# Optimization experiments

Measured on AMD Instinct MI355X. Metric: run time of the kernel, lower is better.

Reference implementation:

```python
import jax, jax.numpy as jnp
import numpy as np

GROUP_SIZE = 16
E2M1_MAX = 6.0
# Positive E2M1 grid and midpoints for round-to-nearest
E2M1_POS = jnp.array([0.0, 0.5, 1.0, 1.5, 2.0, 3.0, 4.0, 6.0], jnp.float32)
E2M1_MID = jnp.array([0.25, 0.75, 1.25, 1.75, 2.5, 3.5, 5.0], jnp.float32)
# Full 16-entry signed LUT (bit3 = sign, sign-magnitude)
E2M1_LUT = jnp.array([0.0, 0.5, 1.0, 1.5, 2.0, 3.0, 4.0, 6.0,
                      -0.0, -0.5, -1.0, -1.5, -2.0, -3.0, -4.0, -6.0], jnp.float32)

def _round_e2m1(x):
    # nearest value on the E2M1 grid (clamped to +-6)
    idx = jnp.searchsorted(E2M1_MID, jnp.abs(x))
    return jnp.sign(x) * E2M1_POS[idx]

def nvfp4_act_qdq(x, input_scale):
    # per-group dynamic quantize to NVFP4 with fp8-e4m3 group scale, then dequantize
    orig_shape = x.shape
    xg = x.astype(jnp.float32).reshape(*orig_shape[:-1], -1, GROUP_SIZE)
    amax = jnp.max(jnp.abs(xg), axis=-1, keepdims=True)
    s = (amax / (E2M1_MAX * input_scale)).astype(jnp.float8_e4m3fn).astype(jnp.float32)
    s = jnp.where(s > 0, s, 1.0)
    total = s * input_scale  # effective per-group scale
    dq = _round_e2m1(xg / total) * total
    return dq.reshape(orig_shape).astype(jnp.float16)

def nvfp4_dequantize(weight, weight_scale, weight_scale_2):
    # weight: [O, I//2] packed bytes (values 0..255); low nibble = even index
    O = weight.shape[0]
    low = weight & 0xF
    high = (weight >> 4) & 0xF
    codes = jnp.stack([low, high], axis=-1).reshape(O, -1)  # [O, I]
    vals = E2M1_LUT[codes].reshape(O, -1, GROUP_SIZE)       # [O, G, 16]
    w = vals * weight_scale[:, :, None] * weight_scale_2
    return w.reshape(O, -1).astype(jnp.float16)

def setup_inputs() -> dict:
    key = jax.random.key(0)
    k1, k2, k3 = jax.random.split(key, 3)
    B, S, I, O = 8, 16, 8192, 8192
    hidden_states = jax.random.normal(k1, (B, S, I), dtype=jnp.float16)
    weight = jax.random.randint(k2, (O, I // 2), 0, 256, dtype=jnp.int32)
    weight_scale = jax.random.uniform(k3, (O, I // GROUP_SIZE), dtype=jnp.float32) * 0.05 + 0.001
    weight_scale_2 = jnp.ones((1,), jnp.float32)
    input_scale = jnp.ones((1,), jnp.float32)
    return {"hidden_states": hidden_states, "weight": weight,
            "weight_scale": weight_scale, "weight_scale_2": weight_scale_2,
            "input_scale": input_scale}

def reference(hidden_states, weight, weight_scale, weight_scale_2, input_scale):
    hs_dq = nvfp4_act_qdq(hidden_states, input_scale)
    w_dq = nvfp4_dequantize(weight, weight_scale, weight_scale_2)
    return jnp.matmul(hs_dq, w_dq.T)  # [B, S, O], fp16
```

## Files before the change

kernel.cpp:

```cpp
#include <hip/hip_runtime.h>
#include <stdint.h>


typedef _Float16 half8 __attribute__((ext_vector_type(8)));
typedef float float4v __attribute__((ext_vector_type(4)));

__device__ __forceinline__ uint32_t perm_b32(uint32_t hi, uint32_t lo, uint32_t sel) {
  return __builtin_amdgcn_perm(hi, lo, sel);
}

__device__ __forceinline__ float e4m3_roundtrip(float x) {
  if (x < 0.015625f) {
    return __builtin_rintf(x * 512.0f) * 0.001953125f;
  }
  uint32_t u = __float_as_uint(x);
  u += 0x7FFFFu + ((u >> 20) & 1u);
  u &= 0xFFF00000u;
  float y = __uint_as_float(u);
  return fminf(y, 448.0f);
}

__global__ __launch_bounds__(256)
void aqdq_kernel(const float* __restrict__ hs,
                 const float* __restrict__ isc,
                 uint2* __restrict__ asw) {
  const int t = blockIdx.x * 256 + threadIdx.x;
  const int m = t >> 11;
  const int u = t & 2047;
  const int g = u >> 2;
  const int hq = u & 3;

  const float* p = hs + m * 8192 + g * 16 + hq * 4;
  float4 x = *(const float4*)p;

  float amax = fmaxf(fmaxf(fabsf(x.x), fabsf(x.y)), fmaxf(fabsf(x.z), fabsf(x.w)));
  amax = fmaxf(amax, __shfl_xor(amax, 1));
  amax = fmaxf(amax, __shfl_xor(amax, 2));

  float is = isc[0];
  float s = e4m3_roundtrip(amax / (6.0f * is));
  if (!(s > 0.0f)) s = 1.0f;
  float total = s * is;

  float xv[4] = {x.x, x.y, x.z, x.w};
  union { _Float16 h[4]; uint2 v; } qq;
#pragma unroll
  for (int i = 0; i < 4; ++i) {
    float r = xv[i] / total;
    float a = fabsf(r);
    float v = (a <= 0.25f) ? 0.0f
            : (a <= 0.75f) ? 0.5f
            : (a <= 1.25f) ? 1.0f
            : (a <= 1.75f) ? 1.5f
            : (a <= 2.5f)  ? 2.0f
            : (a <= 3.5f)  ? 3.0f
            : (a <= 5.0f)  ? 4.0f : 6.0f;
    qq.h[i] = (_Float16)(copysignf(v, r) * total);
  }

  const int k = g * 16 + hq * 4;
  const int kb = k >> 5;
  const int quad = (k >> 3) & 3;
  const int lane16 = (m & 15) | (quad << 4);
  const int mb = m >> 4;
  asw[((kb * 8 + mb) * 64 + lane16) * 2 + (hq & 1)] = qq.v;
}

__device__ __forceinline__ half8 decode_scale(int4 w, float sf) {
  uint32_t t0 = perm_b32((uint32_t)w.y, (uint32_t)w.x, 0x00000400u);
  uint32_t t1 = perm_b32((uint32_t)w.w, (uint32_t)w.z, 0x04000000u);
  uint32_t b  = perm_b32(t1, t0, 0x07060100u);
  uint32_t ev = b & 0x0F0F0F0Fu;
  uint32_t od = (b >> 4) & 0x0F0F0F0Fu;
  uint32_t evm = ev & 0x07070707u;
  uint32_t odm = od & 0x07070707u;
  uint32_t evs = (ev & 0x08080808u) << 4;
  uint32_t ods = (od & 0x08080808u) << 4;
  uint32_t evh = perm_b32(0x46444240u, 0x3E3C3800u, evm) | evs;
  uint32_t odh = perm_b32(0x46444240u, 0x3E3C3800u, odm) | ods;
  union { uint32_t u[4]; half8 h; } r;
  r.u[0] = perm_b32(odh, evh, 0x04000000u) & 0xFF00FF00u;
  r.u[1] = perm_b32(odh, evh, 0x05000100u) & 0xFF00FF00u;
  r.u[2] = perm_b32(odh, evh, 0x06000200u) & 0xFF00FF00u;
  r.u[3] = perm_b32(odh, evh, 0x07000300u) & 0xFF00FF00u;
  _Float16 hsf = (_Float16)sf;
  half8 sv = {hsf, hsf, hsf, hsf, hsf, hsf, hsf, hsf};
  return r.h * sv;
}

template<int MODE>
__global__ __launch_bounds__(512, 4)
void gemm_kernel(const uint4* __restrict__ asw,
                 const int* __restrict__ wq,
                 const float* __restrict__ wsc,
                 const float* __restrict__ ws2p,
                 float* __restrict__ dst) {
  __shared__ uint4 abuf[2][8][64];
  const int lane = threadIdx.x & 63;
  const int wv = threadIdx.x >> 6;
  const int quad = lane >> 4;
  const int kp = blockIdx.x & 7;
  const int nb = blockIdx.x >> 3;
  const int col = nb * 128 + wv * 16 + (lane & 15);
  const float ws2 = ws2p[0];
  const int4* wp = (const int4*)(wq + (size_t)col * 4096) + kp * 128 + quad;
  const float2* sp = (const float2*)(wsc + (size_t)col * 512 + kp * 64);
  const uint4* ap = asw + kp * 16384 + wv * 64 + lane;

  float4v acc[8];
#pragma unroll
  for (int mb = 0; mb < 8; ++mb) acc[mb] = (float4v){0.f, 0.f, 0.f, 0.f};

  {
    uint4 a0 = ap[0];
    int4 w0 = wp[0];
    float2 s0 = sp[0];
    abuf[0][wv][lane] = a0;
    __syncthreads();
    int4 wC = w0; float2 sC = s0;
    for (int t = 0; t < 32; ++t) {
      uint4 aN; int4 wN; float2 sN;
      const bool more = (t < 31);
      if (more) {
        aN = ap[(t + 1) * 512];
        wN = wp[(t + 1) * 4];
        sN = sp[t + 1];
      }
      uint4 af[8];
#pragma unroll
      for (int mb = 0; mb < 8; ++mb) af[mb] = abuf[t & 1][mb][lane];
      float sA = ((quad & 2) ? sC.y : sC.x) * ws2;
      half8 bA = decode_scale(wC, sA);
#pragma unroll
      for (int mb = 0; mb < 8; ++mb) {
        union { uint4 u; half8 h; } a;
        a.u = af[mb];
        acc[mb] = __builtin_amdgcn_mfma_f32_16x16x32_f16(a.h, bA, acc[mb], 0, 0, 0);
      }
      if (more) {
        abuf[(t + 1) & 1][wv][lane] = aN;
        __syncthreads();
        wC = wN; sC = sN;
      }
    }
  }

  if (MODE == 0) {
    float* pp = dst + ((size_t)kp << 20) + col;
#pragma unroll
    for (int mb = 0; mb < 8; ++mb) {
      const int mrow = mb * 16 + quad * 4;
#pragma unroll
      for (int r = 0; r < 4; ++r) pp[(size_t)(mrow + r) * 8192] = acc[mb][r];
    }
  } else {
#pragma unroll
    for (int mb = 0; mb < 8; ++mb) {
      const int mrow = mb * 16 + quad * 4;
#pragma unroll
      for (int r = 0; r < 4; ++r)
        unsafeAtomicAdd(&dst[(size_t)(mrow + r) * 8192 + col], acc[mb][r]);
    }
  }
}

__global__ __launch_bounds__(256)
void reduce_kernel(const float4* __restrict__ part, float4* __restrict__ out) {
  const int i = blockIdx.x * 256 + threadIdx.x;
  float4 s = part[i];
#pragma unroll
  for (int p = 1; p < 8; ++p) {
    float4 b = part[(size_t)p * 262144 + i];
    s.x += b.x; s.y += b.y; s.z += b.z; s.w += b.w;
  }
  out[i] = s;
}

extern "C" void kernel_launch(void* const* d_in, const int* in_sizes, int n_in,
                              void* d_out, int out_size, void* d_ws, size_t ws_size,
                              hipStream_t stream) {
  (void)in_sizes; (void)n_in; (void)out_size;
  const float* hs  = (const float*)d_in[0];
  const int* wq    = (const int*)d_in[1];
  const float* wsc = (const float*)d_in[2];
  const float* ws2 = (const float*)d_in[3];
  const float* isc = (const float*)d_in[4];
  float* out       = (float*)d_out;
  uint2* asw2      = (uint2*)d_ws;
  const uint4* asw4 = (const uint4*)d_ws;

  aqdq_kernel<<<1024, 256, 0, stream>>>(hs, isc, asw2);

  const size_t need = ((size_t)2 << 20) + ((size_t)32 << 20);
  if (ws_size >= need) {
    float* part = (float*)((char*)d_ws + ((size_t)2 << 20));
    gemm_kernel<0><<<512, 512, 0, stream>>>(asw4, wq, wsc, ws2, part);
    reduce_kernel<<<1024, 256, 0, stream>>>((const float4*)part, (float4*)out);
  } else {
    hipMemsetAsync(out, 0, (size_t)128 * 8192 * 4, stream);
    gemm_kernel<1><<<512, 512, 0, stream>>>(asw4, wq, wsc, ws2, out);
  }
}
```

Measured before the change: 241.9 us.

## Deepen GEMM prefetch with direct global-to-LDS loads and a 4-stage ring

The activation tiles are now copied straight from global memory into LDS with global_load_lds, so they no longer pass through registers and a separate LDS store. A 4-deep LDS ring with prefetch distance 2 replaces the double buffer, with weights and scales held in a matching register ring. Explicit vmcnt waits and a single barrier per step replace the per-iteration __syncthreads, and the main loop is unrolled by four. The goal is to keep more loads in flight and hide memory latency. The cost is more LDS and registers per block, which may reduce occupancy, and the hand-counted vmcnt values, which must match exactly the number of outstanding loads.

```diff
diff --git a/kernel.cpp b/kernel.cpp
--- a/kernel.cpp
+++ b/kernel.cpp
@@ -7,6 +7,12 @@
 
 __device__ __forceinline__ uint32_t perm_b32(uint32_t hi, uint32_t lo, uint32_t sel) {
   return __builtin_amdgcn_perm(hi, lo, sel);
+}
+
+__device__ __forceinline__ void load_lds16(const uint4* g, uint4* l) {
+  __builtin_amdgcn_global_load_lds((const __attribute__((address_space(1))) void*)g,
+                                   (__attribute__((address_space(3))) void*)l,
+                                   16, 0, 0);
 }
 
 __device__ __forceinline__ float e4m3_roundtrip(float x) {
@@ -95,7 +101,7 @@
                  const float* __restrict__ wsc,
                  const float* __restrict__ ws2p,
                  float* __restrict__ dst) {
-  __shared__ uint4 abuf[2][8][64];
+  __shared__ uint4 abuf[4][8][64];
   const int lane = threadIdx.x & 63;
   const int wv = threadIdx.x >> 6;
   const int quad = lane >> 4;
@@ -111,39 +117,59 @@
 #pragma unroll
   for (int mb = 0; mb < 8; ++mb) acc[mb] = (float4v){0.f, 0.f, 0.f, 0.f};
 
+  int4 wreg[4];
+  float2 sreg[4];
+
+  load_lds16(ap, &abuf[0][wv][0]);
+  wreg[0] = wp[0];
+  sreg[0] = sp[0];
+  load_lds16(ap + 512, &abuf[1][wv][0]);
+  wreg[1] = wp[4];
+  sreg[1] = sp[1];
+
+#define STEP_BODY(J, STAGE_EN, VMCNT_N)                                           \
+  {                                                                               \
+    if (STAGE_EN) {                                                               \
+      load_lds16(apg + ((J) + 2) * 512, &abuf[((J) + 2) & 3][wv][0]);             \
+      wreg[((J) + 2) & 3] = wpg[((J) + 2) * 4];                                   \
+      sreg[((J) + 2) & 3] = spg[(J) + 2];                                         \
+    }                                                                             \
+    __builtin_amdgcn_sched_barrier(0);                                            \
+    asm volatile("s_waitcnt vmcnt(" #VMCNT_N ")" ::: "memory");                   \
+    __builtin_amdgcn_s_barrier();                                                 \
+    __builtin_amdgcn_sched_barrier(0);                                            \
+    uint4 af[8];                                                                  \
+    _Pragma("unroll")                                                             \
+    for (int mb = 0; mb < 8; ++mb) af[mb] = abuf[(J)][mb][lane];                  \
+    float sA = ((quad & 2) ? sreg[(J)].y : sreg[(J)].x) * ws2;                    \
+    half8 bA = decode_scale(wreg[(J)], sA);                                       \
+    _Pragma("unroll")                                                             \
+    for (int mb = 0; mb < 8; ++mb) {                                              \
+      union { uint4 u; half8 h; } a;                                              \
+      a.u = af[mb];                                                               \
+      acc[mb] = __builtin_amdgcn_mfma_f32_16x16x32_f16(a.h, bA, acc[mb], 0, 0, 0);\
+    }                                                                             \
+  }
+
   {
-    uint4 a0 = ap[0];
-    int4 w0 = wp[0];
-    float2 s0 = sp[0];
-    abuf[0][wv][lane] = a0;
-    __syncthreads();
-    int4 wC = w0; float2 sC = s0;
-    for (int t = 0; t < 32; ++t) {
-      uint4 aN; int4 wN; float2 sN;
-      const bool more = (t < 31);
-      if (more) {
-        aN = ap[(t + 1) * 512];
-        wN = wp[(t + 1) * 4];
-        sN = sp[t + 1];
-      }
-      uint4 af[8];
-#pragma unroll
-      for (int mb = 0; mb < 8; ++mb) af[mb] = abuf[t & 1][mb][lane];
-      float sA = ((quad & 2) ? sC.y : sC.x) * ws2;
-      half8 bA = decode_scale(wC, sA);
-#pragma unroll
-      for (int mb = 0; mb < 8; ++mb) {
-        union { uint4 u; half8 h; } a;
-        a.u = af[mb];
-        acc[mb] = __builtin_amdgcn_mfma_f32_16x16x32_f16(a.h, bA, acc[mb], 0, 0, 0);
-      }
-      if (more) {
-        abuf[(t + 1) & 1][wv][lane] = aN;
-        __syncthreads();
-        wC = wN; sC = sN;
-      }
+    const uint4* apg = ap;
+    const int4* wpg = wp;
+    const float2* spg = sp;
+    for (int tt = 0; tt < 28; tt += 4) {
+      STEP_BODY(0, true, 6)
+      STEP_BODY(1, true, 6)
+      STEP_BODY(2, true, 6)
+      STEP_BODY(3, true, 6)
+      apg += 4 * 512;
+      wpg += 16;
+      spg += 4;
     }
-  }
+    STEP_BODY(0, true, 6)
+    STEP_BODY(1, true, 6)
+    STEP_BODY(2, false, 3)
+    STEP_BODY(3, false, 0)
+  }
+#undef STEP_BODY
 
   if (MODE == 0) {
     float* pp = dst + ((size_t)kp << 20) + col;
```

Result: no change. 243.9 us (+0.8%).

## Use direct global-to-LDS loads with 4-step windows and fewer barriers in GEMM

Applied to the files above, without the earlier changes.

Activation tiles now go straight from global memory to LDS through global_load_lds, which drops the register round trip. The K loop is regrouped into 8 windows of 4 k-steps, each with double-buffered weight and scale registers, so there is one barrier per window instead of one per step. Scales are fetched as float4 vectors. In exchange, LDS use grows fourfold and register pressure rises, which could lower occupancy at 512 threads with launch bounds of 4.

```diff
diff --git a/kernel.cpp b/kernel.cpp
--- a/kernel.cpp
+++ b/kernel.cpp
@@ -7,6 +7,12 @@
 
 __device__ __forceinline__ uint32_t perm_b32(uint32_t hi, uint32_t lo, uint32_t sel) {
   return __builtin_amdgcn_perm(hi, lo, sel);
+}
+
+__device__ __forceinline__ void load_lds16(const uint4* g, uint4* l) {
+  __builtin_amdgcn_global_load_lds((const __attribute__((address_space(1))) void*)g,
+                                   (__attribute__((address_space(3))) void*)l,
+                                   16, 0, 0);
 }
 
 __device__ __forceinline__ float e4m3_roundtrip(float x) {
@@ -95,7 +101,7 @@
                  const float* __restrict__ wsc,
                  const float* __restrict__ ws2p,
                  float* __restrict__ dst) {
-  __shared__ uint4 abuf[2][8][64];
+  __shared__ uint4 abuf[2][4][8][64];
   const int lane = threadIdx.x & 63;
   const int wv = threadIdx.x >> 6;
   const int quad = lane >> 4;
@@ -103,47 +109,70 @@
   const int nb = blockIdx.x >> 3;
   const int col = nb * 128 + wv * 16 + (lane & 15);
   const float ws2 = ws2p[0];
-  const int4* wp = (const int4*)(wq + (size_t)col * 4096) + kp * 128 + quad;
-  const float2* sp = (const float2*)(wsc + (size_t)col * 512 + kp * 64);
+  const int4* wp = (const int4*)wq + (size_t)col * 1024 + kp * 128 + quad;
+  const float4v* sp4 = (const float4v*)(wsc + (size_t)col * 512 + kp * 64);
   const uint4* ap = asw + kp * 16384 + wv * 64 + lane;
 
   float4v acc[8];
 #pragma unroll
   for (int mb = 0; mb < 8; ++mb) acc[mb] = (float4v){0.f, 0.f, 0.f, 0.f};
 
-  {
-    uint4 a0 = ap[0];
-    int4 w0 = wp[0];
-    float2 s0 = sp[0];
-    abuf[0][wv][lane] = a0;
-    __syncthreads();
-    int4 wC = w0; float2 sC = s0;
-    for (int t = 0; t < 32; ++t) {
-      uint4 aN; int4 wN; float2 sN;
-      const bool more = (t < 31);
-      if (more) {
-        aN = ap[(t + 1) * 512];
-        wN = wp[(t + 1) * 4];
-        sN = sp[t + 1];
-      }
-      uint4 af[8];
-#pragma unroll
-      for (int mb = 0; mb < 8; ++mb) af[mb] = abuf[t & 1][mb][lane];
-      float sA = ((quad & 2) ? sC.y : sC.x) * ws2;
-      half8 bA = decode_scale(wC, sA);
-#pragma unroll
-      for (int mb = 0; mb < 8; ++mb) {
-        union { uint4 u; half8 h; } a;
-        a.u = af[mb];
-        acc[mb] = __builtin_amdgcn_mfma_f32_16x16x32_f16(a.h, bA, acc[mb], 0, 0, 0);
-      }
-      if (more) {
-        abuf[(t + 1) & 1][wv][lane] = aN;
-        __syncthreads();
-        wC = wN; sC = sN;
-      }
-    }
-  }
+  int4 wA[4], wB[4];
+  float4v sA[2], sB[2];
+
+#pragma unroll
+  for (int s = 0; s < 4; ++s) load_lds16(ap + s * 512, &abuf[0][s][wv][0]);
+#pragma unroll
+  for (int s = 0; s < 4; ++s) wA[s] = wp[s * 4];
+  sA[0] = sp4[0];
+  sA[1] = sp4[1];
+  __builtin_amdgcn_sched_barrier(0);
+  asm volatile("s_waitcnt vmcnt(0)" ::: "memory");
+  __builtin_amdgcn_s_barrier();
+  __builtin_amdgcn_sched_barrier(0);
+
+#define WINDOW(W, WCUR, SCUR, WNXT, SNXT)                                         \
+  {                                                                               \
+    if ((W) < 7) {                                                                \
+      _Pragma("unroll")                                                           \
+      for (int s = 0; s < 4; ++s)                                                 \
+        load_lds16(ap + (((W) + 1) * 4 + s) * 512,                                \
+                   &abuf[((W) + 1) & 1][s][wv][0]);                               \
+      _Pragma("unroll")                                                           \
+      for (int s = 0; s < 4; ++s) WNXT[s] = wp[(((W) + 1) * 4 + s) * 4];          \
+      SNXT[0] = sp4[((W) + 1) * 2];                                               \
+      SNXT[1] = sp4[((W) + 1) * 2 + 1];                                           \
+    }                                                                             \
+    __builtin_amdgcn_sched_barrier(0);                                            \
+    _Pragma("unroll")                                                             \
+    for (int s = 0; s < 4; ++s) {                                                 \
+      uint4 af[8];                                                                \
+      _Pragma("unroll")                                                           \
+      for (int mb = 0; mb < 8; ++mb) af[mb] = abuf[(W) & 1][s][mb][lane];         \
+      float sc = SCUR[s >> 1][(s & 1) * 2 + (quad >> 1)] * ws2;                   \
+      half8 bA = decode_scale(WCUR[s], sc);                                       \
+      _Pragma("unroll")                                                           \
+      for (int mb = 0; mb < 8; ++mb) {                                            \
+        union { uint4 u; half8 h; } a_;                                           \
+        a_.u = af[mb];                                                            \
+        acc[mb] = __builtin_amdgcn_mfma_f32_16x16x32_f16(a_.h, bA, acc[mb], 0, 0, 0); \
+      }                                                                           \
+    }                                                                             \
+    __builtin_amdgcn_sched_barrier(0);                                            \
+    asm volatile("s_waitcnt vmcnt(0)" ::: "memory");                              \
+    __builtin_amdgcn_s_barrier();                                                 \
+    __builtin_amdgcn_sched_barrier(0);                                            \
+  }
+
+  WINDOW(0, wA, sA, wB, sB)
+  WINDOW(1, wB, sB, wA, sA)
+  WINDOW(2, wA, sA, wB, sB)
+  WINDOW(3, wB, sB, wA, sA)
+  WINDOW(4, wA, sA, wB, sB)
+  WINDOW(5, wB, sB, wA, sA)
+  WINDOW(6, wA, sA, wB, sB)
+  WINDOW(7, wB, sB, wA, sA)
+#undef WINDOW
 
   if (MODE == 0) {
     float* pp = dst + ((size_t)kp << 20) + col;
```

After: 229.6 us. 1.05x faster.

## Drop LDS staging, give each wave two column tiles with register prefetch

Applied to the files above, without the earlier changes.

Each wave now computes two 16-column tiles instead of one, so every A fragment loaded from global memory feeds two MFMAs. The shared-memory double buffer and per-step __syncthreads are removed, and each wave reads all 8 A fragments straight from global/L2. The loop is fully unrolled with a 3-deep register prefetch of weights and scales and a 2-deep prefetch of A. The block shrinks to 256 threads at the same grid size, so there are half as many waves. This raises register pressure and global A traffic per wave, and may reduce latency hiding.

```diff
diff --git a/kernel.cpp b/kernel.cpp
--- a/kernel.cpp
+++ b/kernel.cpp
@@ -89,77 +89,90 @@
 }
 
 template<int MODE>
-__global__ __launch_bounds__(512, 4)
+__global__ __launch_bounds__(256, 2)
 void gemm_kernel(const uint4* __restrict__ asw,
                  const int* __restrict__ wq,
                  const float* __restrict__ wsc,
                  const float* __restrict__ ws2p,
                  float* __restrict__ dst) {
-  __shared__ uint4 abuf[2][8][64];
   const int lane = threadIdx.x & 63;
   const int wv = threadIdx.x >> 6;
   const int quad = lane >> 4;
   const int kp = blockIdx.x & 7;
   const int nb = blockIdx.x >> 3;
-  const int col = nb * 128 + wv * 16 + (lane & 15);
+  const int colA = nb * 128 + wv * 32 + (lane & 15);
+  const int colB = colA + 16;
   const float ws2 = ws2p[0];
-  const int4* wp = (const int4*)(wq + (size_t)col * 4096) + kp * 128 + quad;
-  const float2* sp = (const float2*)(wsc + (size_t)col * 512 + kp * 64);
-  const uint4* ap = asw + kp * 16384 + wv * 64 + lane;
-
-  float4v acc[8];
-#pragma unroll
-  for (int mb = 0; mb < 8; ++mb) acc[mb] = (float4v){0.f, 0.f, 0.f, 0.f};
-
-  {
-    uint4 a0 = ap[0];
-    int4 w0 = wp[0];
-    float2 s0 = sp[0];
-    abuf[0][wv][lane] = a0;
-    __syncthreads();
-    int4 wC = w0; float2 sC = s0;
-    for (int t = 0; t < 32; ++t) {
-      uint4 aN; int4 wN; float2 sN;
-      const bool more = (t < 31);
-      if (more) {
-        aN = ap[(t + 1) * 512];
-        wN = wp[(t + 1) * 4];
-        sN = sp[t + 1];
-      }
-      uint4 af[8];
-#pragma unroll
-      for (int mb = 0; mb < 8; ++mb) af[mb] = abuf[t & 1][mb][lane];
-      float sA = ((quad & 2) ? sC.y : sC.x) * ws2;
-      half8 bA = decode_scale(wC, sA);
-#pragma unroll
-      for (int mb = 0; mb < 8; ++mb) {
-        union { uint4 u; half8 h; } a;
-        a.u = af[mb];
-        acc[mb] = __builtin_amdgcn_mfma_f32_16x16x32_f16(a.h, bA, acc[mb], 0, 0, 0);
-      }
-      if (more) {
-        abuf[(t + 1) & 1][wv][lane] = aN;
-        __syncthreads();
-        wC = wN; sC = sN;
-      }
+  const int4* wpA = (const int4*)wq + (size_t)colA * 1024 + kp * 128 + quad;
+  const int4* wpB = (const int4*)wq + (size_t)colB * 1024 + kp * 128 + quad;
+  const float2* spA = (const float2*)(wsc + (size_t)colA * 512 + kp * 64);
+  const float2* spB = (const float2*)(wsc + (size_t)colB * 512 + kp * 64);
+  const uint4* ap = asw + kp * 16384 + lane;
+
+  float4v accA[8], accB[8];
+#pragma unroll
+  for (int mb = 0; mb < 8; ++mb) {
+    accA[mb] = (float4v){0.f, 0.f, 0.f, 0.f};
+    accB[mb] = (float4v){0.f, 0.f, 0.f, 0.f};
+  }
+
+  uint4 af[2][8];
+  int4 wAr[3], wBr[3];
+  float2 sAr[3], sBr[3];
+
+#pragma unroll
+  for (int mb = 0; mb < 8; ++mb) af[0][mb] = ap[mb * 64];
+  wAr[0] = wpA[0];  wBr[0] = wpB[0];
+  sAr[0] = spA[0];  sBr[0] = spB[0];
+  wAr[1] = wpA[4];  wBr[1] = wpB[4];
+  sAr[1] = spA[1];  sBr[1] = spB[1];
+
+#pragma unroll
+  for (int t = 0; t < 32; ++t) {
+    if (t + 2 < 32) {
+      wAr[(t + 2) % 3] = wpA[(t + 2) * 4];
+      wBr[(t + 2) % 3] = wpB[(t + 2) * 4];
+      sAr[(t + 2) % 3] = spA[t + 2];
+      sBr[(t + 2) % 3] = spB[t + 2];
+    }
+    if (t + 1 < 32) {
+#pragma unroll
+      for (int mb = 0; mb < 8; ++mb) af[(t + 1) & 1][mb] = ap[(t + 1) * 512 + mb * 64];
+    }
+    float svA = ((quad & 2) ? sAr[t % 3].y : sAr[t % 3].x) * ws2;
+    float svB = ((quad & 2) ? sBr[t % 3].y : sBr[t % 3].x) * ws2;
+    half8 bA = decode_scale(wAr[t % 3], svA);
+    half8 bB = decode_scale(wBr[t % 3], svB);
+#pragma unroll
+    for (int mb = 0; mb < 8; ++mb) {
+      union { uint4 u; half8 h; } a_;
+      a_.u = af[t & 1][mb];
+      accA[mb] = __builtin_amdgcn_mfma_f32_16x16x32_f16(a_.h, bA, accA[mb], 0, 0, 0);
+      accB[mb] = __builtin_amdgcn_mfma_f32_16x16x32_f16(a_.h, bB, accB[mb], 0, 0, 0);
     }
   }
 
   if (MODE == 0) {
-    float* pp = dst + ((size_t)kp << 20) + col;
+    float* ppA = dst + ((size_t)kp << 20) + colA;
+    float* ppB = dst + ((size_t)kp << 20) + colB;
 #pragma unroll
     for (int mb = 0; mb < 8; ++mb) {
       const int mrow = mb * 16 + quad * 4;
 #pragma unroll
-      for (int r = 0; r < 4; ++r) pp[(size_t)(mrow + r) * 8192] = acc[mb][r];
+      for (int r = 0; r < 4; ++r) {
+        ppA[(size_t)(mrow + r) * 8192] = accA[mb][r];
+        ppB[(size_t)(mrow + r) * 8192] = accB[mb][r];
+      }
     }
   } else {
 #pragma unroll
     for (int mb = 0; mb < 8; ++mb) {
       const int mrow = mb * 16 + quad * 4;
 #pragma unroll
-      for (int r = 0; r < 4; ++r)
-        unsafeAtomicAdd(&dst[(size_t)(mrow + r) * 8192 + col], acc[mb][r]);
+      for (int r = 0; r < 4; ++r) {
+        unsafeAtomicAdd(&dst[(size_t)(mrow + r) * 8192 + colA], accA[mb][r]);
+        unsafeAtomicAdd(&dst[(size_t)(mrow + r) * 8192 + colB], accB[mb][r]);
+      }
     }
   }
 }
@@ -194,10 +207,10 @@
   const size_t need = ((size_t)2 << 20) + ((size_t)32 << 20);
   if (ws_size >= need) {
     float* part = (float*)((char*)d_ws + ((size_t)2 << 20));
-    gemm_kernel<0><<<512, 512, 0, stream>>>(asw4, wq, wsc, ws2, part);
+    gemm_kernel<0><<<512, 256, 0, stream>>>(asw4, wq, wsc, ws2, part);
     reduce_kernel<<<1024, 256, 0, stream>>>((const float4*)part, (float4*)out);
   } else {
     hipMemsetAsync(out, 0, (size_t)128 * 8192 * 4, stream);
-    gemm_kernel<1><<<512, 512, 0, stream>>>(asw4, wq, wsc, ws2, out);
-  }
-}
+    gemm_kernel<1><<<512, 256, 0, stream>>>(asw4, wq, wsc, ws2, out);
+  }
+}
```

Measured after the change: 253.3 us. 1.05x slower.
